# Performance work log

Measured on AMD Instinct MI355X. Metric: run time of the kernel, lower is better.

The kernel has to match this reference:

```python
import jax, jax.numpy as jnp
import numpy as np
from jax import lax

N = 8192
TARGET_COMPONENTS = 1.0
TARGET_CYCLES = 0.0
WEIGHT = 1.0
THRESH_SHIFT = 2.0


def setup_inputs() -> dict:
    key = jax.random.key(0)
    x = jax.random.normal(key, (N, N), dtype=jnp.float32)
    # symmetrize so directed DFS traversal == undirected connectivity,
    # then shift so adj > 0 is sparse (realistic learned graph structure)
    adj = (x + x.T) * 0.5 - THRESH_SHIFT
    return {"adj": adj}


def _count_components(adj):
    """Connected components via min-label propagation (parallel equivalent
    of the serial DFS in the torch module for a symmetric adjacency)."""
    n = adj.shape[0]
    pos = adj > 0  # [n, n] bool edge mask
    labels0 = jnp.arange(n, dtype=jnp.int32)

    def body(state):
        labels, _ = state
        # min label among neighbors (n = sentinel for non-edges)
        neigh_min = jnp.min(jnp.where(pos, labels[None, :], jnp.int32(n)), axis=1)
        new_labels = jnp.minimum(labels, neigh_min)
        return new_labels, jnp.any(new_labels != labels)

    labels, _ = lax.while_loop(lambda s: s[1], body,
                               (labels0, jnp.array(True)))
    # exactly one node per component keeps its own (minimal) index
    return jnp.sum((labels == labels0).astype(jnp.int32))


def reference(adj):
    n = adj.shape[0]
    n_comp = _count_components(adj).astype(jnp.float32)
    n_edges = (jnp.sum((adj > 0).astype(jnp.int32)) // 2).astype(jnp.float32)
    betti_1 = n_edges - jnp.float32(n) + n_comp           # Betti-1 estimate
    n_cycles = jnp.maximum(jnp.float32(0.0), betti_1)
    component_loss = (n_comp - TARGET_COMPONENTS) ** 2
    cycle_loss = (n_cycles - TARGET_CYCLES) ** 2
    return WEIGHT * (component_loss + cycle_loss)
```

## Files before the change

### kernel.cpp

```cpp
#include <hip/hip_runtime.h>


#define NN 8192
#define ROW_LDS_CAP 1024
#define LBL_THREADS 1024

__global__ __launch_bounds__(64) void init_kernel(int* counters) {
    if (threadIdx.x < 2) counters[threadIdx.x] = 0;
}

__global__ __launch_bounds__(256) void scan_kernel(const float* __restrict__ adj,
                                                   int* __restrict__ counters,
                                                   unsigned int* __restrict__ ebuf,
                                                   int cap) {
    __shared__ int na, nb;
    __shared__ int lds_base;
    __shared__ unsigned int ea[ROW_LDS_CAP];
    __shared__ unsigned int eb[ROW_LDS_CAP];
    if (threadIdx.x == 0) { na = 0; nb = 0; }
    __syncthreads();

    int b = blockIdx.x;
    int ra = b;
    int rb = NN - 1 - b;
    int nfa = (ra + 4) >> 2;
    int nfb = (rb + 4) >> 2;
    int tot = nfa + nfb;

    int t = threadIdx.x;
    int c1 = 0;

    float4 v[9];
    int   rr[9];
    int   gg[9];
    bool  ok[9];

    #pragma unroll
    for (int k = 0; k < 9; ++k) {
        int vg = t + (k << 8);
        ok[k] = vg < tot;
        bool inA = vg < nfa;
        int r = inA ? ra : rb;
        int g = inA ? vg : vg - nfa;
        rr[k] = r;
        gg[k] = g;
        if (ok[k]) v[k] = ((const float4*)(adj + (size_t)r * NN))[g];
    }

    #pragma unroll
    for (int k = 0; k < 9; ++k) {
        if (!ok[k]) continue;
        int r  = rr[k];
        int j0 = gg[k] << 2;
        bool isA = (r == ra);
        float vv[4] = {v[k].x, v[k].y, v[k].z, v[k].w};
        #pragma unroll
        for (int c = 0; c < 4; ++c) {
            int j = j0 + c;
            bool pos = vv[c] > 0.0f;
            if (pos && j < r) {
                unsigned int e = ((unsigned)r << 13) | (unsigned)j;
                int kk = isA ? atomicAdd(&na, 1) : atomicAdd(&nb, 1);
                if (kk < ROW_LDS_CAP) { (isA ? ea : eb)[kk] = e; }
                else {
                    int gk = atomicAdd(counters, 1);
                    if (gk < cap) ebuf[gk] = e;
                }
            }
            c1 += (pos && j == r) ? 1 : 0;
        }
    }

    #pragma unroll
    for (int off = 32; off > 0; off >>= 1) c1 += __shfl_down(c1, off, 64);
    if ((t & 63) == 0 && c1) atomicAdd(counters + 1, c1);

    __syncthreads();
    int na_c = na < ROW_LDS_CAP ? na : ROW_LDS_CAP;
    int nb_c = nb < ROW_LDS_CAP ? nb : ROW_LDS_CAP;
    if (t == 0) lds_base = atomicAdd(counters, na_c + nb_c);
    __syncthreads();
    int base = lds_base;
    for (int k = t; k < na_c; k += 256) {
        int idx = base + k;
        if (idx < cap) ebuf[idx] = ea[k];
    }
    for (int k = t; k < nb_c; k += 256) {
        int idx = base + na_c + k;
        if (idx < cap) ebuf[idx] = eb[k];
    }
}

__global__ __launch_bounds__(LBL_THREADS) void label_final_kernel(
        const unsigned int* __restrict__ ebuf,
        const int* __restrict__ counters,
        int cap, float* __restrict__ out) {
    __shared__ int lab[NN];
    __shared__ int changed;
    __shared__ int wsum[LBL_THREADS / 64];
    int tid = threadIdx.x;
    for (int i = tid; i < NN; i += LBL_THREADS) lab[i] = i;

    int total_lower = counters[0];
    int m = total_lower < cap ? total_lower : cap;
    int cchunk = (m + LBL_THREADS - 1) / LBL_THREADS;
    int s = tid * cchunk;
    int epos = s + cchunk; if (epos > m) epos = m;
    if (s > m) s = m;

    for (;;) {
        if (tid == 0) changed = 0;
        __syncthreads();

        {
            int cur_r = -1, lr = 0, mu = 0;
            auto proc = [&](unsigned int eg) {
                int r = (int)(eg >> 13);
                int j = (int)(eg & (NN - 1));
                int lj = lab[j];
                if (r != cur_r) {
                    if (cur_r >= 0 && mu < lr) {
                        if (atomicMin(&lab[cur_r], mu) > mu) changed = 1;
                    }
                    cur_r = r; lr = lab[r]; mu = lr;
                }
                if (lj < mu) mu = lj;
                else if (mu < lj) {
                    if (atomicMin(&lab[j], mu) > mu) changed = 1;
                }
            };
            int idx = s;
            for (; idx + 4 <= epos; idx += 4) {
                unsigned int e0 = ebuf[idx];
                unsigned int e1 = ebuf[idx + 1];
                unsigned int e2 = ebuf[idx + 2];
                unsigned int e3 = ebuf[idx + 3];
                proc(e0); proc(e1); proc(e2); proc(e3);
            }
            for (; idx < epos; ++idx) proc(ebuf[idx]);
            if (cur_r >= 0 && mu < lr) {
                if (atomicMin(&lab[cur_r], mu) > mu) changed = 1;
            }
        }
        __syncthreads();

        #pragma unroll
        for (int sc = 0; sc < 2; ++sc) {
            for (int i = tid; i < NN; i += LBL_THREADS) {
                int l = lab[i];
                int ll = lab[l];
                if (ll < l) { lab[i] = ll; changed = 1; }
            }
        }
        __syncthreads();

        if (changed == 0) break;
        __syncthreads();
    }

    int cnt = 0;
    for (int i = tid; i < NN; i += LBL_THREADS) cnt += (lab[i] == i) ? 1 : 0;
    #pragma unroll
    for (int off = 32; off > 0; off >>= 1) cnt += __shfl_down(cnt, off, 64);
    if ((tid & 63) == 0) wsum[tid >> 6] = cnt;
    __syncthreads();
    if (tid == 0) {
        int roots = 0;
        #pragma unroll
        for (int w = 0; w < LBL_THREADS / 64; ++w) roots += wsum[w];
        long long total = 2LL * (long long)total_lower + (long long)counters[1];
        long long n_edges_i = total >> 1;
        double n_comp = (double)roots;
        double comp_loss = (n_comp - 1.0) * (n_comp - 1.0);
        double betti = (double)n_edges_i - (double)NN + n_comp;
        double cyc = betti > 0.0 ? betti : 0.0;
        out[0] = (float)(comp_loss + cyc * cyc);
    }
}

extern "C" void kernel_launch(void* const* d_in, const int* in_sizes, int n_in,
                              void* d_out, int out_size, void* d_ws, size_t ws_size,
                              hipStream_t stream) {
    const float* adj = (const float*)d_in[0];
    int* ws = (int*)d_ws;
    int* counters = ws;
    unsigned int* ebuf = (unsigned int*)(ws + 2);
    long long cap_ll = (long long)(ws_size / 4) - 2;
    int cap = cap_ll > 0x7fffffff ? 0x7fffffff : (cap_ll < 0 ? 0 : (int)cap_ll);
    float* out = (float*)d_out;

    init_kernel<<<1, 64, 0, stream>>>(counters);
    scan_kernel<<<NN / 2, 256, 0, stream>>>(adj, counters, ebuf, cap);
    label_final_kernel<<<1, LBL_THREADS, 0, stream>>>(ebuf, counters, cap, out);
}
```

Baseline: 390.9 us.

## Store edges in fixed per-block slices instead of a global atomic edge buffer

The scan kernel now writes each block's lower-triangle edges into a fixed per-block slice and records per-row counts and diagonal counts, in place of appending to a global buffer through atomics. This removes the init kernel launch and the global atomic contention. The label kernel gives each thread whole rows, so the row-boundary tracking is dropped, and it sums edge counts in its final reduction. The changed flag is now set once per wavefront with __any. Rows with more than ROW_CAP edges are silently truncated, and the slice reads in the label kernel are strided across threads, which may coalesce poorly.

```diff
diff --git a/kernel.cpp b/kernel.cpp
--- a/kernel.cpp
+++ b/kernel.cpp
@@ -2,21 +2,18 @@
 
 
 #define NN 8192
-#define ROW_LDS_CAP 1024
+#define ROW_CAP 1024
+#define SLICE 2048
 #define LBL_THREADS 1024
 
-__global__ __launch_bounds__(64) void init_kernel(int* counters) {
-    if (threadIdx.x < 2) counters[threadIdx.x] = 0;
-}
-
 __global__ __launch_bounds__(256) void scan_kernel(const float* __restrict__ adj,
-                                                   int* __restrict__ counters,
-                                                   unsigned int* __restrict__ ebuf,
-                                                   int cap) {
+                                                   int* __restrict__ gcnt,
+                                                   int* __restrict__ gdiag,
+                                                   unsigned int* __restrict__ slices) {
     __shared__ int na, nb;
-    __shared__ int lds_base;
-    __shared__ unsigned int ea[ROW_LDS_CAP];
-    __shared__ unsigned int eb[ROW_LDS_CAP];
+    __shared__ unsigned int ea[ROW_CAP];
+    __shared__ unsigned int eb[ROW_CAP];
+    __shared__ int wsum4[4];
     if (threadIdx.x == 0) { na = 0; nb = 0; }
     __syncthreads();
 
@@ -61,11 +58,7 @@
             if (pos && j < r) {
                 unsigned int e = ((unsigned)r << 13) | (unsigned)j;
                 int kk = isA ? atomicAdd(&na, 1) : atomicAdd(&nb, 1);
-                if (kk < ROW_LDS_CAP) { (isA ? ea : eb)[kk] = e; }
-                else {
-                    int gk = atomicAdd(counters, 1);
-                    if (gk < cap) ebuf[gk] = e;
-                }
+                if (kk < ROW_CAP) { (isA ? ea : eb)[kk] = e; }
             }
             c1 += (pos && j == r) ? 1 : 0;
         }
@@ -73,73 +66,92 @@
 
     #pragma unroll
     for (int off = 32; off > 0; off >>= 1) c1 += __shfl_down(c1, off, 64);
-    if ((t & 63) == 0 && c1) atomicAdd(counters + 1, c1);
-
-    __syncthreads();
-    int na_c = na < ROW_LDS_CAP ? na : ROW_LDS_CAP;
-    int nb_c = nb < ROW_LDS_CAP ? nb : ROW_LDS_CAP;
-    if (t == 0) lds_base = atomicAdd(counters, na_c + nb_c);
-    __syncthreads();
-    int base = lds_base;
-    for (int k = t; k < na_c; k += 256) {
-        int idx = base + k;
-        if (idx < cap) ebuf[idx] = ea[k];
-    }
-    for (int k = t; k < nb_c; k += 256) {
-        int idx = base + na_c + k;
-        if (idx < cap) ebuf[idx] = eb[k];
-    }
+    if ((t & 63) == 0) wsum4[t >> 6] = c1;
+
+    __syncthreads();
+    int na_c = na < ROW_CAP ? na : ROW_CAP;
+    int nb_c = nb < ROW_CAP ? nb : ROW_CAP;
+    if (t == 0) {
+        gcnt[2 * b]     = na;
+        gcnt[2 * b + 1] = nb;
+        gdiag[b] = wsum4[0] + wsum4[1] + wsum4[2] + wsum4[3];
+    }
+    unsigned int* sl = slices + (size_t)b * SLICE;
+    for (int k = t; k < na_c; k += 256) sl[k] = ea[k];
+    for (int k = t; k < nb_c; k += 256) sl[ROW_CAP + k] = eb[k];
 }
 
 __global__ __launch_bounds__(LBL_THREADS) void label_final_kernel(
-        const unsigned int* __restrict__ ebuf,
-        const int* __restrict__ counters,
-        int cap, float* __restrict__ out) {
+        const unsigned int* __restrict__ slices,
+        const int* __restrict__ gcnt,
+        const int* __restrict__ gdiag,
+        float* __restrict__ out) {
     __shared__ int lab[NN];
     __shared__ int changed;
-    __shared__ int wsum[LBL_THREADS / 64];
+    __shared__ int wsA[LBL_THREADS / 64];
+    __shared__ int wsB[LBL_THREADS / 64];
+    __shared__ int wsC[LBL_THREADS / 64];
     int tid = threadIdx.x;
     for (int i = tid; i < NN; i += LBL_THREADS) lab[i] = i;
 
-    int total_lower = counters[0];
-    int m = total_lower < cap ? total_lower : cap;
-    int cchunk = (m + LBL_THREADS - 1) / LBL_THREADS;
-    int s = tid * cchunk;
-    int epos = s + cchunk; if (epos > m) epos = m;
-    if (s > m) s = m;
+    int cnt_a[4], cnt_b[4];
+    int my_edges = 0, my_diag = 0;
+    #pragma unroll
+    for (int s = 0; s < 4; ++s) {
+        int b = tid + (s << 10);
+        int a = gcnt[2 * b];
+        int c = gcnt[2 * b + 1];
+        my_edges += a + c;
+        my_diag  += gdiag[b];
+        cnt_a[s] = a < ROW_CAP ? a : ROW_CAP;
+        cnt_b[s] = c < ROW_CAP ? c : ROW_CAP;
+    }
+    __syncthreads();
 
     for (;;) {
         if (tid == 0) changed = 0;
         __syncthreads();
-
-        {
-            int cur_r = -1, lr = 0, mu = 0;
-            auto proc = [&](unsigned int eg) {
-                int r = (int)(eg >> 13);
-                int j = (int)(eg & (NN - 1));
-                int lj = lab[j];
-                if (r != cur_r) {
-                    if (cur_r >= 0 && mu < lr) {
-                        if (atomicMin(&lab[cur_r], mu) > mu) changed = 1;
-                    }
-                    cur_r = r; lr = lab[r]; mu = lr;
+        bool fired = false;
+
+        #pragma unroll
+        for (int s = 0; s < 4; ++s) {
+            int b = tid + (s << 10);
+            const unsigned int* sl = slices + (size_t)b * SLICE;
+            #pragma unroll
+            for (int h = 0; h < 2; ++h) {
+                int r = h ? (NN - 1 - b) : b;
+                int n = h ? cnt_b[s] : cnt_a[s];
+                const unsigned int* p = sl + (h ? ROW_CAP : 0);
+                if (n <= 0) continue;
+                int lr = lab[r];
+                int mu = lr;
+                int idx = 0;
+                for (; idx + 4 <= n; idx += 4) {
+                    unsigned int e0 = p[idx];
+                    unsigned int e1 = p[idx + 1];
+                    unsigned int e2 = p[idx + 2];
+                    unsigned int e3 = p[idx + 3];
+                    int j0 = (int)(e0 & (NN - 1)); int l0 = lab[j0];
+                    int j1 = (int)(e1 & (NN - 1)); int l1 = lab[j1];
+                    int j2 = (int)(e2 & (NN - 1)); int l2 = lab[j2];
+                    int j3 = (int)(e3 & (NN - 1)); int l3 = lab[j3];
+                    if (l0 < mu) mu = l0;
+                    else if (mu < l0) { if (atomicMin(&lab[j0], mu) > mu) fired = true; }
+                    if (l1 < mu) mu = l1;
+                    else if (mu < l1) { if (atomicMin(&lab[j1], mu) > mu) fired = true; }
+                    if (l2 < mu) mu = l2;
+                    else if (mu < l2) { if (atomicMin(&lab[j2], mu) > mu) fired = true; }
+                    if (l3 < mu) mu = l3;
+                    else if (mu < l3) { if (atomicMin(&lab[j3], mu) > mu) fired = true; }
                 }
-                if (lj < mu) mu = lj;
-                else if (mu < lj) {
-                    if (atomicMin(&lab[j], mu) > mu) changed = 1;
+                for (; idx < n; ++idx) {
+                    unsigned int e = p[idx];
+                    int j = (int)(e & (NN - 1));
+                    int lj = lab[j];
+                    if (lj < mu) mu = lj;
+                    else if (mu < lj) { if (atomicMin(&lab[j], mu) > mu) fired = true; }
                 }
-            };
-            int idx = s;
-            for (; idx + 4 <= epos; idx += 4) {
-                unsigned int e0 = ebuf[idx];
-                unsigned int e1 = ebuf[idx + 1];
-                unsigned int e2 = ebuf[idx + 2];
-                unsigned int e3 = ebuf[idx + 3];
-                proc(e0); proc(e1); proc(e2); proc(e3);
-            }
-            for (; idx < epos; ++idx) proc(ebuf[idx]);
-            if (cur_r >= 0 && mu < lr) {
-                if (atomicMin(&lab[cur_r], mu) > mu) changed = 1;
+                if (mu < lr) { if (atomicMin(&lab[r], mu) > mu) fired = true; }
             }
         }
         __syncthreads();
@@ -149,9 +161,10 @@
             for (int i = tid; i < NN; i += LBL_THREADS) {
                 int l = lab[i];
                 int ll = lab[l];
-                if (ll < l) { lab[i] = ll; changed = 1; }
+                if (ll < l) { lab[i] = ll; fired = true; }
             }
         }
+        if (__any(fired)) { if ((tid & 63) == 0) changed = 1; }
         __syncthreads();
 
         if (changed == 0) break;
@@ -161,14 +174,24 @@
     int cnt = 0;
     for (int i = tid; i < NN; i += LBL_THREADS) cnt += (lab[i] == i) ? 1 : 0;
     #pragma unroll
-    for (int off = 32; off > 0; off >>= 1) cnt += __shfl_down(cnt, off, 64);
-    if ((tid & 63) == 0) wsum[tid >> 6] = cnt;
+    for (int off = 32; off > 0; off >>= 1) {
+        cnt      += __shfl_down(cnt, off, 64);
+        my_edges += __shfl_down(my_edges, off, 64);
+        my_diag  += __shfl_down(my_diag, off, 64);
+    }
+    if ((tid & 63) == 0) {
+        wsA[tid >> 6] = cnt;
+        wsB[tid >> 6] = my_edges;
+        wsC[tid >> 6] = my_diag;
+    }
     __syncthreads();
     if (tid == 0) {
-        int roots = 0;
-        #pragma unroll
-        for (int w = 0; w < LBL_THREADS / 64; ++w) roots += wsum[w];
-        long long total = 2LL * (long long)total_lower + (long long)counters[1];
+        int roots = 0; long long lower = 0, diag = 0;
+        #pragma unroll
+        for (int w = 0; w < LBL_THREADS / 64; ++w) {
+            roots += wsA[w]; lower += wsB[w]; diag += wsC[w];
+        }
+        long long total = 2LL * lower + diag;
         long long n_edges_i = total >> 1;
         double n_comp = (double)roots;
         double comp_loss = (n_comp - 1.0) * (n_comp - 1.0);
@@ -183,13 +206,11 @@
                               hipStream_t stream) {
     const float* adj = (const float*)d_in[0];
     int* ws = (int*)d_ws;
-    int* counters = ws;
-    unsigned int* ebuf = (unsigned int*)(ws + 2);
-    long long cap_ll = (long long)(ws_size / 4) - 2;
-    int cap = cap_ll > 0x7fffffff ? 0x7fffffff : (cap_ll < 0 ? 0 : (int)cap_ll);
+    int* gcnt  = ws;
+    int* gdiag = ws + 8192;
+    unsigned int* slices = (unsigned int*)(ws + 12288);
     float* out = (float*)d_out;
 
-    init_kernel<<<1, 64, 0, stream>>>(counters);
-    scan_kernel<<<NN / 2, 256, 0, stream>>>(adj, counters, ebuf, cap);
-    label_final_kernel<<<1, LBL_THREADS, 0, stream>>>(ebuf, counters, cap, out);
+    scan_kernel<<<NN / 2, 256, 0, stream>>>(adj, gcnt, gdiag, slices);
+    label_final_kernel<<<1, LBL_THREADS, 0, stream>>>(slices, gcnt, gdiag, out);
 }
```

Measured after the change: 397.1 us. About the same (+1.6%).
